# Performance work log

Hardware: AMD Instinct MI355X
Metric: run time of the kernel (lower is better)

Reference implementation:

```python
import jax, jax.numpy as jnp
import numpy as np

B, N, D = 4, 4096, 64
TAU_FLOW, TAU_COLOR, TAU_PROX = 0.8, 0.7, 0.5
GAMMA, ETA, NU = 5.0, 1.0, 1.0
SIGMA = 0.1  # default sigma in calculate_proximity_similarity


def setup_inputs() -> dict:
    key = jax.random.key(0)
    k1, k2, k3, k4 = jax.random.split(key, 4)
    flow = jax.random.normal(k1, (B, N, 3), dtype=jnp.float32)
    color = jax.random.uniform(k2, (B, N, 3), dtype=jnp.float32) * 255.0  # raw 0-255 colors
    coord = jax.random.normal(k3, (B, N, 3), dtype=jnp.float32)
    features = jax.random.normal(k4, (B, N, D), dtype=jnp.float32)
    return {"flow": flow, "color": color, "coord": coord, "features": features}


def _cdist(x):
    # batched pairwise euclidean distance: [B,N,d] -> [B,N,N]
    sq = jnp.sum(x * x, axis=-1)
    d2 = sq[:, :, None] + sq[:, None, :] - 2.0 * jnp.einsum('bnd,bmd->bnm', x, x)
    return jnp.sqrt(jnp.maximum(d2, 0.0))


def _contrast_loss(features, sim, tau):
    # within_sample_contrastive_loss + compute_contrastive_loss (score_higher_positive=True)
    fn = features / (jnp.linalg.norm(features, axis=-1, keepdims=True) + 1e-7)
    fs = jnp.einsum('bnd,bmd->bnm', fn, fn)  # feature cosine similarity [B,N,N]
    g_plus = jax.nn.sigmoid(GAMMA * (sim - tau))   # 1/(1+exp(gamma*(tau-s)))
    g_minus = jax.nn.sigmoid(GAMMA * (tau - sim))  # 1/(1+exp(gamma*(s-tau)))
    s_plus_exp = jnp.sum(jnp.exp(ETA * fs * g_plus), axis=-1)    # [B,N]
    s_minus_exp = jnp.sum(jnp.exp(-NU * fs * g_minus), axis=-1)  # [B,N]
    loss_per_point = jnp.log1p(s_plus_exp) / ETA + jnp.log1p(s_minus_exp) / NU
    # mean over points per sample, then mean over batch, negated
    return -jnp.mean(loss_per_point)


def reference(flow, color, coord, features):
    # flow cosine similarity
    fnorm = jnp.linalg.norm(flow, axis=-1)
    flow_sim = jnp.einsum('bnd,bmd->bnm', flow, flow) / (fnorm[:, :, None] * fnorm[:, None, :] + 1e-8)
    # color similarity: 1 - normalized cdist on colors/255
    c = color / 255.0
    color_sim = 1.0 - _cdist(c) / jnp.sqrt(jnp.float32(color.shape[-1]))
    # proximity similarity: exp(-d / (2*sigma^2))
    prox_sim = jnp.exp(-_cdist(coord) / (2.0 * SIGMA ** 2))
    loss = (1.0 * _contrast_loss(features, flow_sim, TAU_FLOW)
            + 1.0 * _contrast_loss(features, color_sim, TAU_COLOR)
            + 1.0 * _contrast_loss(features, prox_sim, TAU_PROX))
    return loss
```

## Files before the change

kernel.cpp:

```cpp
#include <hip/hip_runtime.h>
#include <math.h>

#define B_ 4
#define N_ 4096
#define BN_ (B_*N_)
#define NT 64
#define NCH 2

typedef __bf16 v8bf __attribute__((ext_vector_type(8)));
typedef unsigned short u16x8 __attribute__((ext_vector_type(8)));
typedef float v4f __attribute__((ext_vector_type(4)));
typedef float v2f __attribute__((ext_vector_type(2)));

#define LOG2E 1.44269504088896340736f
#define CPROX (-50.0f*LOG2E)
#define INVSQRT3 0.57735026918962576f
#define GS (1.0f/1.4f)
#define GC_FLOW  (0.5f - 0.8f*GS)
#define GC_COLOR (0.5f - 0.7f*GS)
#define GC_PROX  (0.5f - 0.5f*GS)
#define D2P_MIN 0.09f

__device__ __forceinline__ float fexp2(float x){ return __builtin_amdgcn_exp2f(x); }
__device__ __forceinline__ float fsqrt(float x){ return __builtin_amdgcn_sqrtf(x); }

#define PKGATE(s2_, gcv_, SPA, SMA, CPA, CPB)                          \
  { v2f t_ = s2_*GSv + gcv_;                                           \
    t_ = __builtin_elementwise_max(t_, zerov);                         \
    t_ = __builtin_elementwise_min(t_, onev);                          \
    v2f t2_ = t_*t_;                                                   \
    v2f u_  = t_*m2v + c3v;                                            \
    v2f a_  = (t2_*u_)*fsl;                                            \
    v2f e1_ = {fexp2(a_.x), fexp2(a_.y)};                              \
    v2f e2_ = E2*e1_;                                                  \
    SPA += e1_; SMA += e2_; CPA += e1_; CPB += e2_; }

extern "C" __global__ __launch_bounds__(256) void prep_k(
    const float* __restrict__ flow, const float* __restrict__ color,
    const float* __restrict__ coord, const float* __restrict__ feat,
    unsigned short* __restrict__ fn, float* __restrict__ scal)
{
  const int wave = blockIdx.x*4 + (threadIdx.x>>6);
  const int lane = threadIdx.x & 63;
  float v = feat[(size_t)wave*64 + lane];
  float ss = v*v;
  #pragma unroll
  for (int d=32; d; d>>=1) ss += __shfl_xor(ss, d);
  float sc = 1.0f/(sqrtf(ss)+1e-7f);
  float x = v*sc;
  unsigned u = __builtin_bit_cast(unsigned, x);
  unsigned r = (u + 0x7fffu + ((u>>16)&1u)) >> 16;
  fn[(size_t)wave*64+lane] = (unsigned short)r;
  if (lane==0) {
    float fx=flow[wave*3+0], fy=flow[wave*3+1], fz=flow[wave*3+2];
    float rn = 1.0f/sqrtf(fx*fx+fy*fy+fz*fz + 1e-8f);
    const float k = 1.0f/255.0f;
    float cx=color[wave*3+0]*k, cy=color[wave*3+1]*k, cz=color[wave*3+2]*k;
    float px=coord[wave*3+0], py=coord[wave*3+1], pz=coord[wave*3+2];
    float* o = scal + (size_t)wave*12;
    o[0]=fx*rn; o[1]=fy*rn; o[2]=fz*rn;
    o[3]=cx; o[4]=cy; o[5]=cz;
    o[6]=cx*cx+cy*cy+cz*cz;
    o[7]=px; o[8]=py; o[9]=pz;
    o[10]=px*px+py*py+pz*pz;
    o[11]=0.f;
  }
}

extern "C" __global__ __launch_bounds__(256,2) void main_k(
    const unsigned short* __restrict__ fn, const float* __restrict__ scal,
    float* __restrict__ part_row, float* __restrict__ part2)
{
  __shared__ unsigned short fnj[2][64*64];
  __shared__ float scj[2][64*12];
  __shared__ float colacc[2][4][64][6];

  const int ti = blockIdx.x & 63;
  const int k  = blockIdx.x >> 6;
  const int b  = blockIdx.y;
  const int c0 = k*17;
  const int npt = 17 - k;

  const int tid  = threadIdx.x;
  const int w    = tid >> 6;
  const int lane = tid & 63;
  const int g    = lane >> 4;
  const int col  = lane & 15;
  const int irow0 = ti*64 + w*16;

  const unsigned short* fnb = fn + (size_t)b*N_*64;
  const float* scb = scal + (size_t)b*N_*12;

  const int srow = tid>>3, sseg = tid&7;
  const int ssw  = (srow&7)<<4;
  const int scrow = tid/3, scseg = tid-3*(tid/3);

  const int arow = irow0 + col;
  v8bf a0 = __builtin_bit_cast(v8bf, *(const u16x8*)(fnb + (size_t)arow*64 + g*8));
  v8bf a1 = __builtin_bit_cast(v8bf, *(const u16x8*)(fnb + (size_t)arow*64 + 32 + g*8));

  v2f fhi[2][3], ci2[2][3], pi2[2][3];
  #pragma unroll
  for (int rp=0;rp<2;++rp) {
    const float* sA = scb + (size_t)(irow0 + g*4 + 2*rp)*12;
    const float* sB = sA + 12;
    v4f a0s = *(const v4f*)(sA), a1s = *(const v4f*)(sA+4), a2s = *(const v4f*)(sA+8);
    v4f b0s = *(const v4f*)(sB), b1s = *(const v4f*)(sB+4), b2s = *(const v4f*)(sB+8);
    fhi[rp][0] = (v2f){a0s.x, b0s.x}; fhi[rp][1] = (v2f){a0s.y, b0s.y}; fhi[rp][2] = (v2f){a0s.z, b0s.z};
    ci2[rp][0] = (v2f){a0s.w, b0s.w}; ci2[rp][1] = (v2f){a1s.x, b1s.x}; ci2[rp][2] = (v2f){a1s.y, b1s.y};
    pi2[rp][0] = (v2f){a1s.w, b1s.w}; pi2[rp][1] = (v2f){a2s.x, b2s.x}; pi2[rp][2] = (v2f){a2s.y, b2s.y};
  }

  const v2f zerov = {0.f,0.f}, onev = {1.f,1.f};
  const v2f GSv = {GS,GS}, m2v = {-2.f,-2.f}, c3v = {3.f,3.f};
  const v2f gcF = {GC_FLOW,GC_FLOW}, gcC = {GC_COLOR,GC_COLOR}, gcP = {GC_PROX,GC_PROX};
  const v2f l2e = {LOG2E,LOG2E}, cprx = {CPROX,CPROX}, nis3 = {-INVSQRT3,-INVSQRT3};

  v2f spa2[3][2], sma2[3][2];
  #pragma unroll
  for (int l=0;l<3;++l)
    #pragma unroll
    for (int rp=0;rp<2;++rp){ spa2[l][rp]=zerov; sma2[l][rp]=zerov; }

  {
    const int tj = (ti + c0) & 63;
    const unsigned short* fng = fnb + (size_t)tj*4096;
    const float* scg = scb + (size_t)tj*768;
    float4 f0 = *(const float4*)(fng + (size_t)srow*64 + sseg*8);
    float4 f1 = *(const float4*)(fng + (size_t)(srow+32)*64 + sseg*8);
    *(float4*)((char*)fnj[0] + srow*128 + ((sseg*16)^ssw)) = f0;
    *(float4*)((char*)fnj[0] + (srow+32)*128 + ((sseg*16)^ssw)) = f1;
    if (tid < 192)
      *(float4*)(scj[0] + scrow*12 + scseg*4) = *(const float4*)(scg + (size_t)scrow*12 + scseg*4);
  }
  __syncthreads();

  int cprev=-1, tjprev=0;
  for (int t2=0; t2<npt; ++t2) {
    const int p  = t2&1;
    const int c  = c0 + t2;
    const int tj = (ti + c) & 63;
    const bool docol = (c>=1 && c<=31);
    const bool more  = (t2<npt-1);

    float4 f0, f1, sv;
    if (more) {
      const int tjn = (ti + c + 1) & 63;
      const unsigned short* fng = fnb + (size_t)tjn*4096;
      const float* scg = scb + (size_t)tjn*768;
      f0 = *(const float4*)(fng + (size_t)srow*64 + sseg*8);
      f1 = *(const float4*)(fng + (size_t)(srow+32)*64 + sseg*8);
      if (tid < 192) sv = *(const float4*)(scg + (size_t)scrow*12 + scseg*4);
    }

    if (t2>0 && cprev>=1 && cprev<=31) {
      const int pp = p^1;
      for (int s=tid; s<384; s+=256) {
        int jl=s/6, kk=s-6*jl;
        float v = colacc[pp][0][jl][kk]+colacc[pp][1][jl][kk]
                + colacc[pp][2][jl][kk]+colacc[pp][3][jl][kk];
        part2[(((size_t)b*31 + (cprev-1))*N_ + tjprev*64 + jl)*6 + kk] = v;
      }
    }

    #pragma unroll
    for (int sub=0; sub<4; ++sub) {
      const int jloc = sub*16 + col;
      const int sw = (jloc&7)<<4;
      const char* rowp = (const char*)fnj[p] + jloc*128;
      v8bf b0 = __builtin_bit_cast(v8bf, *(const u16x8*)(rowp + ((g*16) ^ sw)));
      v8bf b1 = __builtin_bit_cast(v8bf, *(const u16x8*)(rowp + ((64 + g*16) ^ sw)));
      v4f j0 = *(const v4f*)(scj[p] + jloc*12);
      v4f j1 = *(const v4f*)(scj[p] + jloc*12 + 4);
      v4f j2 = *(const v4f*)(scj[p] + jloc*12 + 8);

      v4f acc = {0.f,0.f,0.f,0.f};
      acc = __builtin_amdgcn_mfma_f32_16x16x32_bf16(a0, b0, acc, 0,0,0);
      acc = __builtin_amdgcn_mfma_f32_16x16x32_bf16(a1, b1, acc, 0,0,0);

      const v2f jf0={j0.x,j0.x}, jf1={j0.y,j0.y}, jf2={j0.z,j0.z};
      const v2f jc0={j0.w,j0.w}, jc1={j1.x,j1.x}, jc2={j1.y,j1.y};
      const v2f jp0={j1.w,j1.w}, jp1={j2.x,j2.x}, jp2={j2.y,j2.y};

      v2f cp0=zerov, cp1=zerov, cp2=zerov, cp3=zerov, cp4=zerov, cp5=zerov;

      #pragma unroll
      for (int rp=0;rp<2;++rp) {
        const v2f fs = {acc[2*rp], acc[2*rp+1]};
        const v2f sf = fhi[rp][0]*jf0 + fhi[rp][1]*jf1 + fhi[rp][2]*jf2;
        v2f dc0 = ci2[rp][0]-jc0, dc1 = ci2[rp][1]-jc1, dc2 = ci2[rp][2]-jc2;
        v2f d2c = dc0*dc0 + dc1*dc1 + dc2*dc2;
        v2f sq_c = {fsqrt(d2c.x), fsqrt(d2c.y)};
        const v2f scl = sq_c*nis3 + onev;
        v2f dp0 = pi2[rp][0]-jp0, dp1 = pi2[rp][1]-jp1, dp2 = pi2[rp][2]-jp2;
        v2f d2p = dp0*dp0 + dp1*dp1 + dp2*dp2;
        v2f spr;
        if (__any(__builtin_fminf(d2p.x, d2p.y) < D2P_MIN)) {
          v2f sq_p = {fsqrt(d2p.x), fsqrt(d2p.y)};
          v2f pa = sq_p*cprx;
          spr = (v2f){fexp2(pa.x), fexp2(pa.y)};
        } else {
          spr = zerov;
        }
        const v2f fsl = fs*l2e;
        const v2f nfsl = zerov - fsl;
        const v2f E2 = {fexp2(nfsl.x), fexp2(nfsl.y)};
        PKGATE(sf,  gcF, spa2[0][rp], sma2[0][rp], cp0, cp1);
        PKGATE(scl, gcC, spa2[1][rp], sma2[1][rp], cp2, cp3);
        PKGATE(spr, gcP, spa2[2][rp], sma2[2][rp], cp4, cp5);
      }

      if (docol) {
        float h0 = cp0.x+cp0.y, h1 = cp1.x+cp1.y, h2 = cp2.x+cp2.y;
        float h3 = cp3.x+cp3.y, h4 = cp4.x+cp4.y, h5 = cp5.x+cp5.y;
        h0 += __shfl_xor(h0,16); h0 += __shfl_xor(h0,32);
        h1 += __shfl_xor(h1,16); h1 += __shfl_xor(h1,32);
        h2 += __shfl_xor(h2,16); h2 += __shfl_xor(h2,32);
        h3 += __shfl_xor(h3,16); h3 += __shfl_xor(h3,32);
        h4 += __shfl_xor(h4,16); h4 += __shfl_xor(h4,32);
        h5 += __shfl_xor(h5,16); h5 += __shfl_xor(h5,32);
        if (lane < 16) {
          float* ca = colacc[p][w][jloc];
          ca[0]=h0; ca[1]=h1; ca[2]=h2; ca[3]=h3; ca[4]=h4; ca[5]=h5;
        }
      }
    }

    if (more) {
      const int nb = p^1;
      *(float4*)((char*)fnj[nb] + srow*128 + ((sseg*16)^ssw)) = f0;
      *(float4*)((char*)fnj[nb] + (srow+32)*128 + ((sseg*16)^ssw)) = f1;
      if (tid < 192) *(float4*)(scj[nb] + scrow*12 + scseg*4) = sv;
    }

    __syncthreads();
    cprev=c; tjprev=tj;
  }

  if (cprev>=1 && cprev<=31) {
    const int pl = (npt-1)&1;
    for (int s=tid; s<384; s+=256) {
      int jl=s/6, kk=s-6*jl;
      float v = colacc[pl][0][jl][kk]+colacc[pl][1][jl][kk]
              + colacc[pl][2][jl][kk]+colacc[pl][3][jl][kk];
      part2[(((size_t)b*31 + (cprev-1))*N_ + tjprev*64 + jl)*6 + kk] = v;
    }
  }

  float spa[3][4], sma[3][4];
  #pragma unroll
  for (int l=0;l<3;++l)
    #pragma unroll
    for (int rp=0;rp<2;++rp) {
      spa[l][2*rp]=spa2[l][rp].x; spa[l][2*rp+1]=spa2[l][rp].y;
      sma[l][2*rp]=sma2[l][rp].x; sma[l][2*rp+1]=sma2[l][rp].y;
    }
  #pragma unroll
  for (int l=0;l<3;++l)
    #pragma unroll
    for (int r=0;r<4;++r) {
      float a=spa[l][r], cc=sma[l][r];
      #pragma unroll
      for (int d=1; d<16; d<<=1){ a += __shfl_xor(a,d); cc += __shfl_xor(cc,d); }
      spa[l][r]=a; sma[l][r]=cc;
    }
  if (col==0) {
    #pragma unroll
    for (int r=0;r<4;++r) {
      float* o = part_row + (((size_t)b*NCH + k)*N_ + irow0 + g*4 + r)*6;
      o[0]=spa[0][r]; o[1]=sma[0][r];
      o[2]=spa[1][r]; o[3]=sma[1][r];
      o[4]=spa[2][r]; o[5]=sma[2][r];
    }
  }
}

extern "C" __global__ __launch_bounds__(256) void fin1_k(
    const float* __restrict__ part_row, const float* __restrict__ part2,
    float* __restrict__ partial)
{
  const int pt = blockIdx.x*256 + threadIdx.x;
  const int b = pt >> 12;
  const int i = pt & (N_-1);
  float s[6] = {0.f,0.f,0.f,0.f,0.f,0.f};
  #pragma unroll
  for (int kc=0;kc<NCH;++kc) {
    const float* pp = part_row + (((size_t)b*NCH + kc)*N_ + i)*6;
    #pragma unroll
    for (int q=0;q<6;++q) s[q] += pp[q];
  }
  for (int c=1;c<=31;++c) {
    const float* pp = part2 + (((size_t)b*31 + (c-1))*N_ + i)*6;
    #pragma unroll
    for (int q=0;q<6;++q) s[q] += pp[q];
  }
  float acc = log1pf(s[0]) + log1pf(s[1]) + log1pf(s[2])
            + log1pf(s[3]) + log1pf(s[4]) + log1pf(s[5]);
  #pragma unroll
  for (int d=32; d; d>>=1) acc += __shfl_xor(acc, d);
  __shared__ float wsum[4];
  if ((threadIdx.x&63)==0) wsum[threadIdx.x>>6] = acc;
  __syncthreads();
  if (threadIdx.x==0) partial[blockIdx.x] = wsum[0]+wsum[1]+wsum[2]+wsum[3];
}

extern "C" __global__ void fin2_k(const float* __restrict__ partial, float* __restrict__ out)
{
  float acc = partial[threadIdx.x];
  #pragma unroll
  for (int d=32; d; d>>=1) acc += __shfl_xor(acc, d);
  if (threadIdx.x==0) out[0] = -acc * (1.0f/(float)BN_);
}

extern "C" void kernel_launch(void* const* d_in, const int* in_sizes, int n_in,
                              void* d_out, int out_size, void* d_ws, size_t ws_size,
                              hipStream_t stream)
{
  const float* flow  = (const float*)d_in[0];
  const float* color = (const float*)d_in[1];
  const float* coord = (const float*)d_in[2];
  const float* feat  = (const float*)d_in[3];
  char* ws = (char*)d_ws;
  unsigned short* fn = (unsigned short*)ws;
  float* scal     = (float*)(ws + 2097152);
  float* part_row = (float*)(ws + 2883584);
  float* part2    = (float*)(ws + 3670016);
  float* partial  = (float*)(ws + 15859712);
  float* outp = (float*)d_out;
  hipLaunchKernelGGL(prep_k, dim3(BN_/4), dim3(256), 0, stream,
                     flow, color, coord, feat, fn, scal);
  hipLaunchKernelGGL(main_k, dim3(NT*NCH, B_), dim3(256), 0, stream,
                     fn, scal, part_row, part2);
  hipLaunchKernelGGL(fin1_k, dim3(BN_/256), dim3(256), 0, stream,
                     part_row, part2, partial);
  hipLaunchKernelGGL(fin2_k, dim3(1), dim3(64), 0, stream, partial, outp);
}
```

Before: 95.81 us.

## Process two column tiles per barrier phase and rebalance tile split

The main kernel's j-tile loop now handles two 64-column tiles per phase. Shared buffers are double-buffered across phases, so the number of __syncthreads and column-partial flushes is roughly halved. The split between the two chunks changes from 17/16 tiles to 16/17, so block k=1 gets the extra tile. The finalize kernels are also reshaped: fin1 uses 256 small 64-thread blocks and fin2 reduces 256 partials. The cost is doubled LDS use (fnj, scj and colacc), which may reduce occupancy below the two blocks per CU that launch_bounds requests.

Measured after the change: 94.86 us. Within noise of the previous version (-1.0%).

```diff
diff --git a/kernel.cpp b/kernel.cpp
--- a/kernel.cpp
+++ b/kernel.cpp
@@ -34,6 +34,20 @@
     v2f e1_ = {fexp2(a_.x), fexp2(a_.y)};                              \
     v2f e2_ = E2*e1_;                                                  \
     SPA += e1_; SMA += e2_; CPA += e1_; CPB += e2_; }
+
+#define FLUSHP(par_, base_, cnt_)                                                 \
+  for (int s_=0; s_<(cnt_); ++s_) {                                               \
+    const int cf_ = (base_) + s_;                                                 \
+    if (cf_>=1 && cf_<=31) {                                                      \
+      const int tjf_ = (ti + cf_) & 63;                                           \
+      for (int x_=tid; x_<384; x_+=256) {                                         \
+        int jl_=x_/6, kk_=x_-6*jl_;                                               \
+        float v_ = colacc[par_][s_][0][jl_][kk_]+colacc[par_][s_][1][jl_][kk_]    \
+                 + colacc[par_][s_][2][jl_][kk_]+colacc[par_][s_][3][jl_][kk_];   \
+        part2[(((size_t)b*31 + (cf_-1))*N_ + tjf_*64 + jl_)*6 + kk_] = v_;        \
+      }                                                                           \
+    }                                                                             \
+  }
 
 extern "C" __global__ __launch_bounds__(256) void prep_k(
     const float* __restrict__ flow, const float* __restrict__ color,
@@ -71,15 +85,17 @@
     const unsigned short* __restrict__ fn, const float* __restrict__ scal,
     float* __restrict__ part_row, float* __restrict__ part2)
 {
-  __shared__ unsigned short fnj[2][64*64];
-  __shared__ float scj[2][64*12];
-  __shared__ float colacc[2][4][64][6];
+  __shared__ unsigned short fnj[2][2][64*64];
+  __shared__ float scj[2][2][64*12];
+  __shared__ float colacc[2][2][4][64][6];
 
   const int ti = blockIdx.x & 63;
   const int k  = blockIdx.x >> 6;
   const int b  = blockIdx.y;
-  const int c0 = k*17;
-  const int npt = 17 - k;
+  const int c0 = k*16;
+  const int npt = 16 + k;
+  const int nphase = (npt + 1) >> 1;
+  const int ph0cnt = (npt & 1) ? 1 : 2;
 
   const int tid  = threadIdx.x;
   const int w    = tid >> 6;
@@ -122,130 +138,123 @@
     #pragma unroll
     for (int rp=0;rp<2;++rp){ spa2[l][rp]=zerov; sma2[l][rp]=zerov; }
 
-  {
-    const int tj = (ti + c0) & 63;
+  for (int s=0; s<ph0cnt; ++s) {
+    const int tj = (ti + c0 + s) & 63;
     const unsigned short* fng = fnb + (size_t)tj*4096;
     const float* scg = scb + (size_t)tj*768;
     float4 f0 = *(const float4*)(fng + (size_t)srow*64 + sseg*8);
     float4 f1 = *(const float4*)(fng + (size_t)(srow+32)*64 + sseg*8);
-    *(float4*)((char*)fnj[0] + srow*128 + ((sseg*16)^ssw)) = f0;
-    *(float4*)((char*)fnj[0] + (srow+32)*128 + ((sseg*16)^ssw)) = f1;
+    *(float4*)((char*)fnj[0][s] + srow*128 + ((sseg*16)^ssw)) = f0;
+    *(float4*)((char*)fnj[0][s] + (srow+32)*128 + ((sseg*16)^ssw)) = f1;
     if (tid < 192)
-      *(float4*)(scj[0] + scrow*12 + scseg*4) = *(const float4*)(scg + (size_t)scrow*12 + scseg*4);
+      *(float4*)(scj[0][s] + scrow*12 + scseg*4) = *(const float4*)(scg + (size_t)scrow*12 + scseg*4);
   }
   __syncthreads();
 
-  int cprev=-1, tjprev=0;
-  for (int t2=0; t2<npt; ++t2) {
-    const int p  = t2&1;
-    const int c  = c0 + t2;
-    const int tj = (ti + c) & 63;
-    const bool docol = (c>=1 && c<=31);
-    const bool more  = (t2<npt-1);
-
-    float4 f0, f1, sv;
-    if (more) {
-      const int tjn = (ti + c + 1) & 63;
-      const unsigned short* fng = fnb + (size_t)tjn*4096;
-      const float* scg = scb + (size_t)tjn*768;
-      f0 = *(const float4*)(fng + (size_t)srow*64 + sseg*8);
-      f1 = *(const float4*)(fng + (size_t)(srow+32)*64 + sseg*8);
-      if (tid < 192) sv = *(const float4*)(scg + (size_t)scrow*12 + scseg*4);
-    }
-
-    if (t2>0 && cprev>=1 && cprev<=31) {
-      const int pp = p^1;
-      for (int s=tid; s<384; s+=256) {
-        int jl=s/6, kk=s-6*jl;
-        float v = colacc[pp][0][jl][kk]+colacc[pp][1][jl][kk]
-                + colacc[pp][2][jl][kk]+colacc[pp][3][jl][kk];
-        part2[(((size_t)b*31 + (cprev-1))*N_ + tjprev*64 + jl)*6 + kk] = v;
+  int cbase = c0, cnt = ph0cnt;
+  int pbase = 0, pcnt = 0;
+  for (int ph = 0; ph < nphase; ++ph) {
+    const int p  = ph & 1;
+    const int pn = p ^ 1;
+    const int cnt_next = (ph+1 < nphase) ? 2 : 0;
+    const int cbase_next = cbase + cnt;
+
+    if (pcnt) { FLUSHP(pn, pbase, pcnt); }
+
+    const int smax = cnt > cnt_next ? cnt : cnt_next;
+    for (int s = 0; s < smax; ++s) {
+      float4 f0, f1, sv;
+      const bool doload = s < cnt_next;
+      if (doload) {
+        const int tjn = (ti + cbase_next + s) & 63;
+        const unsigned short* fng = fnb + (size_t)tjn*4096;
+        const float* scg = scb + (size_t)tjn*768;
+        f0 = *(const float4*)(fng + (size_t)srow*64 + sseg*8);
+        f1 = *(const float4*)(fng + (size_t)(srow+32)*64 + sseg*8);
+        if (tid < 192) sv = *(const float4*)(scg + (size_t)scrow*12 + scseg*4);
+      }
+
+      if (s < cnt) {
+        const int c  = cbase + s;
+        const bool docol = (c>=1 && c<=31);
+
+        #pragma unroll
+        for (int sub=0; sub<4; ++sub) {
+          const int jloc = sub*16 + col;
+          const int sw = (jloc&7)<<4;
+          const char* rowp = (const char*)fnj[p][s] + jloc*128;
+          v8bf b0 = __builtin_bit_cast(v8bf, *(const u16x8*)(rowp + ((g*16) ^ sw)));
+          v8bf b1 = __builtin_bit_cast(v8bf, *(const u16x8*)(rowp + ((64 + g*16) ^ sw)));
+          v4f j0 = *(const v4f*)(scj[p][s] + jloc*12);
+          v4f j1 = *(const v4f*)(scj[p][s] + jloc*12 + 4);
+          v4f j2 = *(const v4f*)(scj[p][s] + jloc*12 + 8);
+
+          v4f acc = {0.f,0.f,0.f,0.f};
+          acc = __builtin_amdgcn_mfma_f32_16x16x32_bf16(a0, b0, acc, 0,0,0);
+          acc = __builtin_amdgcn_mfma_f32_16x16x32_bf16(a1, b1, acc, 0,0,0);
+
+          const v2f jf0={j0.x,j0.x}, jf1={j0.y,j0.y}, jf2={j0.z,j0.z};
+          const v2f jc0={j0.w,j0.w}, jc1={j1.x,j1.x}, jc2={j1.y,j1.y};
+          const v2f jp0={j1.w,j1.w}, jp1={j2.x,j2.x}, jp2={j2.y,j2.y};
+
+          v2f cp0=zerov, cp1=zerov, cp2=zerov, cp3=zerov, cp4=zerov, cp5=zerov;
+
+          #pragma unroll
+          for (int rp=0;rp<2;++rp) {
+            const v2f fs = {acc[2*rp], acc[2*rp+1]};
+            const v2f sf = fhi[rp][0]*jf0 + fhi[rp][1]*jf1 + fhi[rp][2]*jf2;
+            v2f dc0 = ci2[rp][0]-jc0, dc1 = ci2[rp][1]-jc1, dc2 = ci2[rp][2]-jc2;
+            v2f d2c = dc0*dc0 + dc1*dc1 + dc2*dc2;
+            v2f sq_c = {fsqrt(d2c.x), fsqrt(d2c.y)};
+            const v2f scl = sq_c*nis3 + onev;
+            v2f dp0 = pi2[rp][0]-jp0, dp1 = pi2[rp][1]-jp1, dp2 = pi2[rp][2]-jp2;
+            v2f d2p = dp0*dp0 + dp1*dp1 + dp2*dp2;
+            v2f spr;
+            if (__any(__builtin_fminf(d2p.x, d2p.y) < D2P_MIN)) {
+              v2f sq_p = {fsqrt(d2p.x), fsqrt(d2p.y)};
+              v2f pa = sq_p*cprx;
+              spr = (v2f){fexp2(pa.x), fexp2(pa.y)};
+            } else {
+              spr = zerov;
+            }
+            const v2f fsl = fs*l2e;
+            const v2f nfsl = zerov - fsl;
+            const v2f E2 = {fexp2(nfsl.x), fexp2(nfsl.y)};
+            PKGATE(sf,  gcF, spa2[0][rp], sma2[0][rp], cp0, cp1);
+            PKGATE(scl, gcC, spa2[1][rp], sma2[1][rp], cp2, cp3);
+            PKGATE(spr, gcP, spa2[2][rp], sma2[2][rp], cp4, cp5);
+          }
+
+          if (docol) {
+            float h0 = cp0.x+cp0.y, h1 = cp1.x+cp1.y, h2 = cp2.x+cp2.y;
+            float h3 = cp3.x+cp3.y, h4 = cp4.x+cp4.y, h5 = cp5.x+cp5.y;
+            h0 += __shfl_xor(h0,16); h0 += __shfl_xor(h0,32);
+            h1 += __shfl_xor(h1,16); h1 += __shfl_xor(h1,32);
+            h2 += __shfl_xor(h2,16); h2 += __shfl_xor(h2,32);
+            h3 += __shfl_xor(h3,16); h3 += __shfl_xor(h3,32);
+            h4 += __shfl_xor(h4,16); h4 += __shfl_xor(h4,32);
+            h5 += __shfl_xor(h5,16); h5 += __shfl_xor(h5,32);
+            if (lane < 16) {
+              float* ca = colacc[p][s][w][jloc];
+              ca[0]=h0; ca[1]=h1; ca[2]=h2; ca[3]=h3; ca[4]=h4; ca[5]=h5;
+            }
+          }
+        }
+      }
+
+      if (doload) {
+        *(float4*)((char*)fnj[pn][s] + srow*128 + ((sseg*16)^ssw)) = f0;
+        *(float4*)((char*)fnj[pn][s] + (srow+32)*128 + ((sseg*16)^ssw)) = f1;
+        if (tid < 192) *(float4*)(scj[pn][s] + scrow*12 + scseg*4) = sv;
       }
     }
 
-    #pragma unroll
-    for (int sub=0; sub<4; ++sub) {
-      const int jloc = sub*16 + col;
-      const int sw = (jloc&7)<<4;
-      const char* rowp = (const char*)fnj[p] + jloc*128;
-      v8bf b0 = __builtin_bit_cast(v8bf, *(const u16x8*)(rowp + ((g*16) ^ sw)));
-      v8bf b1 = __builtin_bit_cast(v8bf, *(const u16x8*)(rowp + ((64 + g*16) ^ sw)));
-      v4f j0 = *(const v4f*)(scj[p] + jloc*12);
-      v4f j1 = *(const v4f*)(scj[p] + jloc*12 + 4);
-      v4f j2 = *(const v4f*)(scj[p] + jloc*12 + 8);
-
-      v4f acc = {0.f,0.f,0.f,0.f};
-      acc = __builtin_amdgcn_mfma_f32_16x16x32_bf16(a0, b0, acc, 0,0,0);
-      acc = __builtin_amdgcn_mfma_f32_16x16x32_bf16(a1, b1, acc, 0,0,0);
-
-      const v2f jf0={j0.x,j0.x}, jf1={j0.y,j0.y}, jf2={j0.z,j0.z};
-      const v2f jc0={j0.w,j0.w}, jc1={j1.x,j1.x}, jc2={j1.y,j1.y};
-      const v2f jp0={j1.w,j1.w}, jp1={j2.x,j2.x}, jp2={j2.y,j2.y};
-
-      v2f cp0=zerov, cp1=zerov, cp2=zerov, cp3=zerov, cp4=zerov, cp5=zerov;
-
-      #pragma unroll
-      for (int rp=0;rp<2;++rp) {
-        const v2f fs = {acc[2*rp], acc[2*rp+1]};
-        const v2f sf = fhi[rp][0]*jf0 + fhi[rp][1]*jf1 + fhi[rp][2]*jf2;
-        v2f dc0 = ci2[rp][0]-jc0, dc1 = ci2[rp][1]-jc1, dc2 = ci2[rp][2]-jc2;
-        v2f d2c = dc0*dc0 + dc1*dc1 + dc2*dc2;
-        v2f sq_c = {fsqrt(d2c.x), fsqrt(d2c.y)};
-        const v2f scl = sq_c*nis3 + onev;
-        v2f dp0 = pi2[rp][0]-jp0, dp1 = pi2[rp][1]-jp1, dp2 = pi2[rp][2]-jp2;
-        v2f d2p = dp0*dp0 + dp1*dp1 + dp2*dp2;
-        v2f spr;
-        if (__any(__builtin_fminf(d2p.x, d2p.y) < D2P_MIN)) {
-          v2f sq_p = {fsqrt(d2p.x), fsqrt(d2p.y)};
-          v2f pa = sq_p*cprx;
-          spr = (v2f){fexp2(pa.x), fexp2(pa.y)};
-        } else {
-          spr = zerov;
-        }
-        const v2f fsl = fs*l2e;
-        const v2f nfsl = zerov - fsl;
-        const v2f E2 = {fexp2(nfsl.x), fexp2(nfsl.y)};
-        PKGATE(sf,  gcF, spa2[0][rp], sma2[0][rp], cp0, cp1);
-        PKGATE(scl, gcC, spa2[1][rp], sma2[1][rp], cp2, cp3);
-        PKGATE(spr, gcP, spa2[2][rp], sma2[2][rp], cp4, cp5);
-      }
-
-      if (docol) {
-        float h0 = cp0.x+cp0.y, h1 = cp1.x+cp1.y, h2 = cp2.x+cp2.y;
-        float h3 = cp3.x+cp3.y, h4 = cp4.x+cp4.y, h5 = cp5.x+cp5.y;
-        h0 += __shfl_xor(h0,16); h0 += __shfl_xor(h0,32);
-        h1 += __shfl_xor(h1,16); h1 += __shfl_xor(h1,32);
-        h2 += __shfl_xor(h2,16); h2 += __shfl_xor(h2,32);
-        h3 += __shfl_xor(h3,16); h3 += __shfl_xor(h3,32);
-        h4 += __shfl_xor(h4,16); h4 += __shfl_xor(h4,32);
-        h5 += __shfl_xor(h5,16); h5 += __shfl_xor(h5,32);
-        if (lane < 16) {
-          float* ca = colacc[p][w][jloc];
-          ca[0]=h0; ca[1]=h1; ca[2]=h2; ca[3]=h3; ca[4]=h4; ca[5]=h5;
-        }
-      }
-    }
-
-    if (more) {
-      const int nb = p^1;
-      *(float4*)((char*)fnj[nb] + srow*128 + ((sseg*16)^ssw)) = f0;
-      *(float4*)((char*)fnj[nb] + (srow+32)*128 + ((sseg*16)^ssw)) = f1;
-      if (tid < 192) *(float4*)(scj[nb] + scrow*12 + scseg*4) = sv;
-    }
-
     __syncthreads();
-    cprev=c; tjprev=tj;
-  }
-
-  if (cprev>=1 && cprev<=31) {
-    const int pl = (npt-1)&1;
-    for (int s=tid; s<384; s+=256) {
-      int jl=s/6, kk=s-6*jl;
-      float v = colacc[pl][0][jl][kk]+colacc[pl][1][jl][kk]
-              + colacc[pl][2][jl][kk]+colacc[pl][3][jl][kk];
-      part2[(((size_t)b*31 + (cprev-1))*N_ + tjprev*64 + jl)*6 + kk] = v;
-    }
-  }
+    pbase = cbase; pcnt = cnt;
+    cbase = cbase_next; cnt = cnt_next;
+  }
+
+  { const int pl = (nphase-1)&1; FLUSHP(pl, pbase, pcnt); }
 
   float spa[3][4], sma[3][4];
   #pragma unroll
@@ -275,11 +284,11 @@
   }
 }
 
-extern "C" __global__ __launch_bounds__(256) void fin1_k(
+extern "C" __global__ __launch_bounds__(64) void fin1_k(
     const float* __restrict__ part_row, const float* __restrict__ part2,
     float* __restrict__ partial)
 {
-  const int pt = blockIdx.x*256 + threadIdx.x;
+  const int pt = blockIdx.x*64 + threadIdx.x;
   const int b = pt >> 12;
   const int i = pt & (N_-1);
   float s[6] = {0.f,0.f,0.f,0.f,0.f,0.f};
@@ -298,18 +307,19 @@
             + log1pf(s[3]) + log1pf(s[4]) + log1pf(s[5]);
   #pragma unroll
   for (int d=32; d; d>>=1) acc += __shfl_xor(acc, d);
+  if (threadIdx.x==0) partial[blockIdx.x] = acc;
+}
+
+extern "C" __global__ void fin2_k(const float* __restrict__ partial, float* __restrict__ out)
+{
+  const int tid = threadIdx.x;
+  float acc = partial[tid];
+  #pragma unroll
+  for (int d=32; d; d>>=1) acc += __shfl_xor(acc, d);
   __shared__ float wsum[4];
-  if ((threadIdx.x&63)==0) wsum[threadIdx.x>>6] = acc;
+  if ((tid&63)==0) wsum[tid>>6] = acc;
   __syncthreads();
-  if (threadIdx.x==0) partial[blockIdx.x] = wsum[0]+wsum[1]+wsum[2]+wsum[3];
-}
-
-extern "C" __global__ void fin2_k(const float* __restrict__ partial, float* __restrict__ out)
-{
-  float acc = partial[threadIdx.x];
-  #pragma unroll
-  for (int d=32; d; d>>=1) acc += __shfl_xor(acc, d);
-  if (threadIdx.x==0) out[0] = -acc * (1.0f/(float)BN_);
+  if (tid==0) out[0] = -(wsum[0]+wsum[1]+wsum[2]+wsum[3]) * (1.0f/(float)BN_);
 }
 
 extern "C" void kernel_launch(void* const* d_in, const int* in_sizes, int n_in,
@@ -331,7 +341,7 @@
                      flow, color, coord, feat, fn, scal);
   hipLaunchKernelGGL(main_k, dim3(NT*NCH, B_), dim3(256), 0, stream,
                      fn, scal, part_row, part2);
-  hipLaunchKernelGGL(fin1_k, dim3(BN_/256), dim3(256), 0, stream,
+  hipLaunchKernelGGL(fin1_k, dim3(BN_/64), dim3(64), 0, stream,
                      part_row, part2, partial);
-  hipLaunchKernelGGL(fin2_k, dim3(1), dim3(64), 0, stream, partial, outp);
-}
+  hipLaunchKernelGGL(fin2_k, dim3(1), dim3(256), 0, stream, partial, outp);
+}
```
